# Kernel tuning notes

Measured on AMD Instinct MI355X. Metric: run time of the kernel, lower is better.

The kernel has to match this reference:

```python
import jax, jax.numpy as jnp
import numpy as np

NEG = -1e9

def setup_inputs() -> dict:
    key = jax.random.key(0)
    kx, kq, kk, kv, kbq, kbk, kbv = jax.random.split(key, 7)
    B, S, E, D = 4, 2048, 1024, 64
    x = jax.random.normal(kx, (B, S, E), dtype=jnp.float32)
    # causal mask, broadcast over batch (mask == 0 positions get -1e9)
    mask = jnp.broadcast_to(jnp.tril(jnp.ones((S, S), dtype=jnp.int32)), (B, S, S))
    scale = 1.0 / np.sqrt(E)
    Wq = jax.random.normal(kq, (E, D), dtype=jnp.float32) * scale
    Wk = jax.random.normal(kk, (E, D), dtype=jnp.float32) * scale
    Wv = jax.random.normal(kv, (E, D), dtype=jnp.float32) * scale
    bq = jnp.zeros((D,), dtype=jnp.float32)
    bk = jnp.zeros((D,), dtype=jnp.float32)
    bv = jnp.zeros((D,), dtype=jnp.float32)
    return {"x": x, "mask": mask, "Wq": Wq, "bq": bq, "Wk": Wk, "bk": bk, "Wv": Wv, "bv": bv}

def reference(x, mask, Wq, bq, Wk, bk, Wv, bv):
    # Faithful to original: forward passes (K(x), Q(x), V(x)) into sdpa,
    # so the K-projection plays the 'query' role and Q-projection the 'key' role.
    q = jnp.einsum('bse,ed->bsd', x, Wk) + bk  # K(x) used as queries
    k = jnp.einsum('bse,ed->bsd', x, Wq) + bq  # Q(x) used as keys
    v = jnp.einsum('bse,ed->bsd', x, Wv) + bv
    d = q.shape[-1]
    scores = jnp.einsum('bsd,btd->bst', q, k) / jnp.sqrt(jnp.asarray(d, q.dtype))
    scores = jnp.where(mask == 0, jnp.asarray(NEG, scores.dtype), scores)
    weights = jax.nn.softmax(scores, axis=-1)
    return jnp.einsum('bst,btd->bsd', weights, v)
```

## Files before the change

### kernel.cpp

```cpp
#include <hip/hip_runtime.h>

typedef short bf16x8 __attribute__((ext_vector_type(8)));
typedef float f32x4  __attribute__((ext_vector_type(4)));
typedef int   i32x4  __attribute__((ext_vector_type(4)));

#define NEG_BIG (-1e9f)

__device__ __forceinline__ float bf2f(unsigned short h){
  union { unsigned u; float f; } v; v.u = ((unsigned)h) << 16; return v.f;
}
__device__ __forceinline__ unsigned short f2bf(float f){
  union { float f; unsigned u; } v; v.f = f;
  unsigned u = v.u;
  return (unsigned short)((u + 0x7FFFu + ((u >> 16) & 1u)) >> 16);
}

__global__ __launch_bounds__(256) void prep_kernel(
    const float* __restrict__ Wq, const float* __restrict__ bq,
    const float* __restrict__ Wk, const float* __restrict__ bk,
    const float* __restrict__ Wv, const float* __restrict__ bv,
    unsigned short* __restrict__ Wimg, float* __restrict__ bias)
{
  __shared__ float Wt[64][65];

  const int tid = threadIdx.x;
  const int kb2 = blockIdx.x / 6;
  const int rem = blockIdx.x % 6;
  const int mat = rem >> 1;
  const int kh  = rem & 1;
  const int kbase = kb2 * 128 + kh * 64;

  const float* W = (mat == 0) ? Wk : (mat == 1) ? Wq : Wv;

  #pragma unroll
  for (int i = 0; i < 4; i++) {
    int krow = (tid >> 4) + i * 16;
    int d4   = (tid & 15) * 4;
    f32x4 v = *(const f32x4*)&W[(size_t)(kbase + krow) * 64 + d4];
    Wt[krow][d4 + 0] = v[0];
    Wt[krow][d4 + 1] = v[1];
    Wt[krow][d4 + 2] = v[2];
    Wt[krow][d4 + 3] = v[3];
  }
  __syncthreads();

  const int d = tid >> 2;
  const int c = tid & 3;
  const int r = mat * 64 + d;
  #pragma unroll
  for (int h = 0; h < 2; h++) {
    int cc = c + h * 4;
    bf16x8 o;
    #pragma unroll
    for (int i = 0; i < 8; i++) o[i] = f2bf(Wt[cc * 8 + i][d]);
    *(bf16x8*)&Wimg[(size_t)kb2 * 24576 + r * 128 + kh * 64 + cc * 8] = o;
  }

  if (blockIdx.x == 0 && tid < 192) {
    float b;
    if (tid < 64)       b = bk[tid];
    else if (tid < 128) b = bq[tid - 64];
    else                b = bv[tid - 128];
    bias[tid] = b;
  }
}

__global__ __launch_bounds__(256, 2) void proj_kernel(
    const float* __restrict__ x,
    const unsigned short* __restrict__ Wimg,
    const float* __restrict__ bias,
    unsigned short* __restrict__ Qh,
    unsigned short* __restrict__ Kh, unsigned short* __restrict__ Vth)
{
  __shared__ __align__(16) unsigned short Axb[32 * 128];
  __shared__ __align__(16) unsigned short Wc[96 * 128];

  const int tid  = threadIdx.x;
  const int lane = tid & 63;
  const int w    = tid >> 6;
  const int rh   = w & 1;
  const int cg   = w >> 1;
  const int quad = lane >> 4;
  const int li   = lane & 15;
  const int rowbase = (blockIdx.x >> 1) * 32;
  const int ch      = blockIdx.x & 1;

  const int xr0 = tid >> 4,          xc0 = tid & 15;
  const int xr1 = (tid + 256) >> 4,  xc1 = tid & 15;
  const float* agp0 = x + (size_t)(rowbase + xr0) * 1024 + xc0 * 8;
  const float* agp1 = x + (size_t)(rowbase + xr1) * 1024 + xc1 * 8;
  const int aslot0 = xr0 * 128 + (xc0 ^ (xr0 & 15)) * 8;
  const int aslot1 = xr1 * 128 + (xc1 ^ (xr1 & 15)) * 8;

  int wslot[6];
  const unsigned short* wgp[6];
  #pragma unroll
  for (int j = 0; j < 6; j++) {
    int cid = tid + j * 256;
    int wr = cid >> 4, c = cid & 15;
    wslot[j] = wr * 128 + (c ^ (wr & 15)) * 8;
    wgp[j] = Wimg + (size_t)(ch * 96 + wr) * 128 + c * 8;
  }

  f32x4 acc[3];
  #pragma unroll
  for (int c = 0; c < 3; c++) acc[c] = (f32x4){0.f, 0.f, 0.f, 0.f};

  const int alr = rh * 16 + li;

  f32x4 rA[4];
  rA[0] = *(const f32x4*)(agp0);
  rA[1] = *(const f32x4*)(agp0 + 4);
  rA[2] = *(const f32x4*)(agp1);
  rA[3] = *(const f32x4*)(agp1 + 4);
  i32x4 rW[6];
  #pragma unroll
  for (int j = 0; j < 6; j++) rW[j] = *(const i32x4*)(wgp[j]);

  for (int ks = 0; ks < 8; ks++) {
    bf16x8 xa, xb;
    #pragma unroll
    for (int j = 0; j < 4; j++) {
      xa[j]     = f2bf(rA[0][j]);
      xa[4 + j] = f2bf(rA[1][j]);
      xb[j]     = f2bf(rA[2][j]);
      xb[4 + j] = f2bf(rA[3][j]);
    }
    __syncthreads();
    *(bf16x8*)&Axb[aslot0] = xa;
    *(bf16x8*)&Axb[aslot1] = xb;
    #pragma unroll
    for (int j = 0; j < 6; j++) *(i32x4*)&Wc[wslot[j]] = rW[j];
    if (ks < 7) {
      rA[0] = *(const f32x4*)(agp0 + (ks + 1) * 128);
      rA[1] = *(const f32x4*)(agp0 + (ks + 1) * 128 + 4);
      rA[2] = *(const f32x4*)(agp1 + (ks + 1) * 128);
      rA[3] = *(const f32x4*)(agp1 + (ks + 1) * 128 + 4);
      #pragma unroll
      for (int j = 0; j < 6; j++)
        rW[j] = *(const i32x4*)(wgp[j] + (size_t)(ks + 1) * 24576);
    }
    __syncthreads();

    #pragma unroll
    for (int sub = 0; sub < 4; sub++) {
      bf16x8 af = *(const bf16x8*)&Axb[alr * 128 + ((sub * 4 + quad) ^ (alr & 15)) * 8];
      #pragma unroll
      for (int ct = 0; ct < 3; ct++) {
        const int lw = cg * 48 + ct * 16 + li;
        bf16x8 bf = *(const bf16x8*)&Wc[lw * 128 + ((sub * 4 + quad) ^ (lw & 15)) * 8];
        acc[ct] = __builtin_amdgcn_mfma_f32_16x16x32_bf16(af, bf, acc[ct], 0, 0, 0);
      }
    }
  }

  if (ch == 0) {
    #pragma unroll
    for (int ct = 0; ct < 3; ct++)
      #pragma unroll
      for (int r = 0; r < 4; r++) {
        int row = rowbase + rh * 16 + quad * 4 + r;
        int col = cg * 48 + ct * 16 + li;
        unsigned short h = f2bf(acc[ct][r] + bias[col]);
        if (col < 64) Qh[(size_t)row * 64 + col] = h;
        else          Kh[(size_t)row * 64 + (col - 64)] = h;
      }
  } else {
    __syncthreads();
    unsigned short* Vlds = Wc;
    #pragma unroll
    for (int ct = 0; ct < 3; ct++)
      #pragma unroll
      for (int r = 0; r < 4; r++) {
        int srow = rh * 16 + quad * 4 + r;
        int col = 96 + cg * 48 + ct * 16 + li;
        unsigned short h = f2bf(acc[ct][r] + bias[col]);
        if (col < 128) Kh[(size_t)(rowbase + srow) * 64 + (col - 64)] = h;
        else           Vlds[(col - 128) * 40 + srow] = h;
      }
    __syncthreads();
    const int d  = tid >> 2;
    const int sc = tid & 3;
    bf16x8 vv = *(const bf16x8*)&Vlds[d * 40 + sc * 8];
    const int grow = rowbase;
    const int bb = grow >> 11, s0 = (grow & 2047) + sc * 8;
    *(bf16x8*)&Vth[(size_t)bb * 131072 + (size_t)d * 2048 + s0] = vv;
  }
}

__global__ __launch_bounds__(256, 3) void attn_part_kernel(
    const unsigned short* __restrict__ Qh,
    const unsigned short* __restrict__ Kh,
    const unsigned short* __restrict__ Vth,
    float* __restrict__ pacc, float* __restrict__ pl,
    float* __restrict__ out)
{
  __shared__ __align__(16) unsigned short Kst[2][64 * 64];
  __shared__ __align__(16) unsigned short Vst[2][64 * 64];
  __shared__ __align__(16) unsigned short Ps[4][16 * 72];

  const int tid  = threadIdx.x;
  const int lane = tid & 63;
  const int w    = tid >> 6;
  const int quad = lane >> 4;
  const int li   = lane & 15;

  const int b = blockIdx.x / 187;
  int r = blockIdx.x % 187;
  int qg = 31, part = 0;
  #pragma unroll 1
  for (int g = 31; g >= 0; g--) {
    int Pg = (g + 3) / 3;
    if (r < Pg) { qg = g; part = r; break; }
    r -= Pg;
  }
  const int nkt = qg + 1;
  const int P   = (qg + 3) / 3;
  const int base = nkt / P, rem = nkt % P;
  const int kt0 = part * base + (part < rem ? part : rem);
  const int kt1 = kt0 + base + (part < rem ? 1 : 0);
  const int qbase = qg * 64 + w * 16;

  size_t qoff = ((size_t)(b * 2048 + qbase) + li) * 64 + quad * 8;
  bf16x8 qh0 = *(const bf16x8*)(Qh + qoff);
  bf16x8 qh1 = *(const bf16x8*)(Qh + qoff + 32);

  f32x4 acc[4];
  #pragma unroll
  for (int c = 0; c < 4; c++) acc[c] = (f32x4){0.f, 0.f, 0.f, 0.f};
  f32x4 lacc = (f32x4){0.f, 0.f, 0.f, 0.f};

  bf16x8 ones;
  #pragma unroll
  for (int j = 0; j < 8; j++) ones[j] = (short)0x3F80;

  const int srow = tid >> 2, sc = tid & 3;
  const unsigned short* kgp = Kh + (size_t)(b * 2048 + srow) * 64 + sc * 8;
  const unsigned short* vgp = Vth + (size_t)b * 131072 + (size_t)srow * 2048 + sc * 8;
  const int ks0 = srow * 64 + ((sc)     ^ (srow & 7)) * 8;
  const int ks1 = srow * 64 + ((sc + 4) ^ (srow & 7)) * 8;

  i32x4 rk0 = *(const i32x4*)(kgp + (size_t)kt0 * 4096);
  i32x4 rk1 = *(const i32x4*)(kgp + (size_t)kt0 * 4096 + 32);
  i32x4 rv0 = *(const i32x4*)(vgp + kt0 * 64);
  i32x4 rv1 = *(const i32x4*)(vgp + kt0 * 64 + 32);

  *(i32x4*)&Kst[0][ks0] = rk0;
  *(i32x4*)&Kst[0][ks1] = rk1;
  *(i32x4*)&Vst[0][ks0] = rv0;
  *(i32x4*)&Vst[0][ks1] = rv1;
  __syncthreads();

  int cur = 0;
  for (int kt = kt0; kt < kt1; kt++) {
    const bool more = (kt + 1 < kt1);
    if (more) {
      rk0 = *(const i32x4*)(kgp + (size_t)(kt + 1) * 4096);
      rk1 = *(const i32x4*)(kgp + (size_t)(kt + 1) * 4096 + 32);
      rv0 = *(const i32x4*)(vgp + (kt + 1) * 64);
      rv1 = *(const i32x4*)(vgp + (kt + 1) * 64 + 32);
    }

    f32x4 s[4];
    #pragma unroll
    for (int c = 0; c < 4; c++) s[c] = (f32x4){0.f, 0.f, 0.f, 0.f};
    __builtin_amdgcn_s_setprio(1);
    #pragma unroll
    for (int ct = 0; ct < 4; ct++) {
      const int n = ct * 16 + li;
      bf16x8 kf0 = *(const bf16x8*)&Kst[cur][n * 64 + ((quad)     ^ (n & 7)) * 8];
      bf16x8 kf1 = *(const bf16x8*)&Kst[cur][n * 64 + ((quad + 4) ^ (n & 7)) * 8];
      s[ct] = __builtin_amdgcn_mfma_f32_16x16x32_bf16(qh0, kf0, s[ct], 0, 0, 0);
      s[ct] = __builtin_amdgcn_mfma_f32_16x16x32_bf16(qh1, kf1, s[ct], 0, 0, 0);
    }
    __builtin_amdgcn_s_setprio(0);

    const bool diag = (kt == qg);
    const int kb = kt * 64;
    #pragma unroll
    for (int ct = 0; ct < 4; ct++)
      #pragma unroll
      for (int rr = 0; rr < 4; rr++) {
        float t = fmaf(s[ct][rr], 0.18033688011112042f, -23.083120654223414f);
        if (diag && (kb + ct * 16 + li > qbase + quad * 4 + rr)) t = -1e30f;
        Ps[w][(quad * 4 + rr) * 72 + ct * 16 + li] = f2bf(exp2f(t));
      }

    bf16x8 ap0 = *(const bf16x8*)&Ps[w][li * 72 + quad * 8];
    bf16x8 ap1 = *(const bf16x8*)&Ps[w][li * 72 + 32 + quad * 8];

    __builtin_amdgcn_s_setprio(1);
    lacc = __builtin_amdgcn_mfma_f32_16x16x32_bf16(ap0, ones, lacc, 0, 0, 0);
    lacc = __builtin_amdgcn_mfma_f32_16x16x32_bf16(ap1, ones, lacc, 0, 0, 0);
    #pragma unroll
    for (int ct = 0; ct < 4; ct++) {
      const int n = ct * 16 + li;
      bf16x8 vf0 = *(const bf16x8*)&Vst[cur][n * 64 + ((quad)     ^ (n & 7)) * 8];
      bf16x8 vf1 = *(const bf16x8*)&Vst[cur][n * 64 + ((quad + 4) ^ (n & 7)) * 8];
      acc[ct] = __builtin_amdgcn_mfma_f32_16x16x32_bf16(ap0, vf0, acc[ct], 0, 0, 0);
      acc[ct] = __builtin_amdgcn_mfma_f32_16x16x32_bf16(ap1, vf1, acc[ct], 0, 0, 0);
    }
    __builtin_amdgcn_s_setprio(0);

    if (more) {
      *(i32x4*)&Kst[cur ^ 1][ks0] = rk0;
      *(i32x4*)&Kst[cur ^ 1][ks1] = rk1;
      *(i32x4*)&Vst[cur ^ 1][ks0] = rv0;
      *(i32x4*)&Vst[cur ^ 1][ks1] = rv1;
      __syncthreads();
      cur ^= 1;
    }
  }

  if (P == 1) {
    float inv[4];
    #pragma unroll
    for (int rr = 0; rr < 4; rr++) inv[rr] = 1.0f / lacc[rr];
    #pragma unroll
    for (int ct = 0; ct < 4; ct++)
      #pragma unroll
      for (int rr = 0; rr < 4; rr++)
        out[(size_t)(b * 2048 + qg * 64 + w * 16 + quad * 4 + rr) * 64 + ct * 16 + li]
          = acc[ct][rr] * inv[rr];
    return;
  }

  const int slot = (b * 32 + qg) * 16 + part;
  float* pa = pacc + (size_t)slot * 4096;
  #pragma unroll
  for (int ct = 0; ct < 4; ct++)
    #pragma unroll
    for (int rr = 0; rr < 4; rr++)
      pa[(w * 16 + quad * 4 + rr) * 64 + ct * 16 + li] = acc[ct][rr];
  if (li == 0) {
    #pragma unroll
    for (int rr = 0; rr < 4; rr++)
      pl[slot * 64 + w * 16 + quad * 4 + rr] = lacc[rr];
  }
}

__global__ __launch_bounds__(256) void attn_merge_kernel(
    const float* __restrict__ pacc, const float* __restrict__ pl,
    float* __restrict__ out)
{
  const int tid = threadIdx.x;
  const int b   = blockIdx.x / 29;
  const int qg  = (blockIdx.x % 29) + 3;
  const int rr  = tid >> 2;
  const int c0  = (tid & 3) * 16;
  const int P   = (qg + 3) / 3;
  const int slot0 = (b * 32 + qg) * 16;

  f32x4 a0 = (f32x4){0.f,0.f,0.f,0.f}, a1 = a0, a2 = a0, a3 = a0;
  float L = 0.f;
  for (int p = 0; p < P; p++) {
    const float* pa = pacc + (size_t)(slot0 + p) * 4096 + rr * 64 + c0;
    a0 += *(const f32x4*)(pa);
    a1 += *(const f32x4*)(pa + 4);
    a2 += *(const f32x4*)(pa + 8);
    a3 += *(const f32x4*)(pa + 12);
    L += pl[(slot0 + p) * 64 + rr];
  }
  float inv = 1.f / L;
  float* o = out + ((size_t)(b * 2048 + qg * 64 + rr)) * 64 + c0;
  *(f32x4*)(o)      = a0 * inv;
  *(f32x4*)(o + 4)  = a1 * inv;
  *(f32x4*)(o + 8)  = a2 * inv;
  *(f32x4*)(o + 12) = a3 * inv;
}

extern "C" void kernel_launch(void* const* d_in, const int* in_sizes, int n_in,
                              void* d_out, int out_size, void* d_ws, size_t ws_size,
                              hipStream_t stream)
{
  (void)in_sizes; (void)n_in; (void)out_size; (void)ws_size;
  const float* x  = (const float*)d_in[0];
  const float* Wq = (const float*)d_in[2];
  const float* bq = (const float*)d_in[3];
  const float* Wk = (const float*)d_in[4];
  const float* bk = (const float*)d_in[5];
  const float* Wv = (const float*)d_in[6];
  const float* bv = (const float*)d_in[7];
  float* out = (float*)d_out;

  char* ws = (char*)d_ws;
  const size_t MB = 1u << 20;
  unsigned short* Qh   = (unsigned short*)(ws);
  unsigned short* Kh   = (unsigned short*)(ws + 2 * MB);
  unsigned short* Vth  = (unsigned short*)(ws + 4 * MB);
  unsigned short* Wimg = (unsigned short*)(ws + 6 * MB);
  float*          bias = (float*)(ws + 6 * MB + 786432);
  float*          pacc = (float*)(ws + 8 * MB);
  float*          pl   = (float*)(ws + 40 * MB);

  prep_kernel<<<dim3(48), dim3(256), 0, stream>>>(Wq, bq, Wk, bk, Wv, bv, Wimg, bias);
  proj_kernel<<<dim3(512), dim3(256), 0, stream>>>(x, Wimg, bias, Qh, Kh, Vth);
  attn_part_kernel<<<dim3(748), dim3(256), 0, stream>>>(Qh, Kh, Vth, pacc, pl, out);
  attn_merge_kernel<<<dim3(116), dim3(256), 0, stream>>>(pacc, pl, out);
}
```

Baseline: 149.9 us.

## Double-buffer projection tiles and load weights directly into LDS

The projection kernel now keeps two LDS buffers for the x and weight tiles, so the next k-step's loads are issued while MFMAs run on the current buffer, with one barrier per step instead of two. Weight tiles move global→LDS through global_load_lds, skipping the register round-trip. Since that instruction cannot swizzle on the way in, the prep kernel now writes the XOR swizzle into the weight image itself. The cost is double the LDS footprint, which may lower occupancy from the requested two blocks per CU, plus reliance on correct ordering and waits for the asynchronous LDS loads.

```diff
diff --git a/kernel.cpp b/kernel.cpp
--- a/kernel.cpp
+++ b/kernel.cpp
@@ -13,6 +13,12 @@
   union { float f; unsigned u; } v; v.f = f;
   unsigned u = v.u;
   return (unsigned short)((u + 0x7FFFu + ((u >> 16) & 1u)) >> 16);
+}
+
+__device__ __forceinline__ void gload_lds16(const unsigned short* g, unsigned short* l){
+  __builtin_amdgcn_global_load_lds(
+      (const __attribute__((address_space(1))) unsigned int*)g,
+      (__attribute__((address_space(3))) unsigned int*)l, 16, 0, 0);
 }
 
 __global__ __launch_bounds__(256) void prep_kernel(
@@ -50,10 +56,12 @@
   #pragma unroll
   for (int h = 0; h < 2; h++) {
     int cc = c + h * 4;
+    int cfull = kh * 8 + cc;
+    int cstore = cfull ^ (r & 15);
     bf16x8 o;
     #pragma unroll
     for (int i = 0; i < 8; i++) o[i] = f2bf(Wt[cc * 8 + i][d]);
-    *(bf16x8*)&Wimg[(size_t)kb2 * 24576 + r * 128 + kh * 64 + cc * 8] = o;
+    *(bf16x8*)&Wimg[(size_t)kb2 * 24576 + r * 128 + cstore * 8] = o;
   }
 
   if (blockIdx.x == 0 && tid < 192) {
@@ -72,8 +80,8 @@
     unsigned short* __restrict__ Qh,
     unsigned short* __restrict__ Kh, unsigned short* __restrict__ Vth)
 {
-  __shared__ __align__(16) unsigned short Axb[32 * 128];
-  __shared__ __align__(16) unsigned short Wc[96 * 128];
+  __shared__ __align__(16) unsigned short Axb[2][32 * 128];
+  __shared__ __align__(16) unsigned short Wc[2][96 * 128];
 
   const int tid  = threadIdx.x;
   const int lane = tid & 63;
@@ -92,15 +100,8 @@
   const int aslot0 = xr0 * 128 + (xc0 ^ (xr0 & 15)) * 8;
   const int aslot1 = xr1 * 128 + (xc1 ^ (xr1 & 15)) * 8;
 
-  int wslot[6];
-  const unsigned short* wgp[6];
-  #pragma unroll
-  for (int j = 0; j < 6; j++) {
-    int cid = tid + j * 256;
-    int wr = cid >> 4, c = cid & 15;
-    wslot[j] = wr * 128 + (c ^ (wr & 15)) * 8;
-    wgp[j] = Wimg + (size_t)(ch * 96 + wr) * 128 + c * 8;
-  }
+  const unsigned short* wtile = Wimg + (size_t)ch * 96 * 128;
+  const int wchunk = w * 64 + lane;
 
   f32x4 acc[3];
   #pragma unroll
@@ -113,11 +114,11 @@
   rA[1] = *(const f32x4*)(agp0 + 4);
   rA[2] = *(const f32x4*)(agp1);
   rA[3] = *(const f32x4*)(agp1 + 4);
-  i32x4 rW[6];
-  #pragma unroll
-  for (int j = 0; j < 6; j++) rW[j] = *(const i32x4*)(wgp[j]);
-
-  for (int ks = 0; ks < 8; ks++) {
+  #pragma unroll
+  for (int j = 0; j < 6; j++)
+    gload_lds16(wtile + (size_t)(j * 256 + wchunk) * 8,
+                &Wc[0][(j * 256 + w * 64) * 8]);
+  {
     bf16x8 xa, xb;
     #pragma unroll
     for (int j = 0; j < 4; j++) {
@@ -126,31 +127,50 @@
       xb[j]     = f2bf(rA[2][j]);
       xb[4 + j] = f2bf(rA[3][j]);
     }
-    __syncthreads();
-    *(bf16x8*)&Axb[aslot0] = xa;
-    *(bf16x8*)&Axb[aslot1] = xb;
-    #pragma unroll
-    for (int j = 0; j < 6; j++) *(i32x4*)&Wc[wslot[j]] = rW[j];
-    if (ks < 7) {
+    *(bf16x8*)&Axb[0][aslot0] = xa;
+    *(bf16x8*)&Axb[0][aslot1] = xb;
+  }
+  __syncthreads();
+
+  int cur = 0;
+  for (int ks = 0; ks < 8; ks++) {
+    const bool more = (ks < 7);
+    if (more) {
+      const unsigned short* wnext = wtile + (size_t)(ks + 1) * 24576;
+      #pragma unroll
+      for (int j = 0; j < 6; j++)
+        gload_lds16(wnext + (size_t)(j * 256 + wchunk) * 8,
+                    &Wc[cur ^ 1][(j * 256 + w * 64) * 8]);
       rA[0] = *(const f32x4*)(agp0 + (ks + 1) * 128);
       rA[1] = *(const f32x4*)(agp0 + (ks + 1) * 128 + 4);
       rA[2] = *(const f32x4*)(agp1 + (ks + 1) * 128);
       rA[3] = *(const f32x4*)(agp1 + (ks + 1) * 128 + 4);
-      #pragma unroll
-      for (int j = 0; j < 6; j++)
-        rW[j] = *(const i32x4*)(wgp[j] + (size_t)(ks + 1) * 24576);
-    }
-    __syncthreads();
+    }
 
     #pragma unroll
     for (int sub = 0; sub < 4; sub++) {
-      bf16x8 af = *(const bf16x8*)&Axb[alr * 128 + ((sub * 4 + quad) ^ (alr & 15)) * 8];
+      bf16x8 af = *(const bf16x8*)&Axb[cur][alr * 128 + ((sub * 4 + quad) ^ (alr & 15)) * 8];
       #pragma unroll
       for (int ct = 0; ct < 3; ct++) {
         const int lw = cg * 48 + ct * 16 + li;
-        bf16x8 bf = *(const bf16x8*)&Wc[lw * 128 + ((sub * 4 + quad) ^ (lw & 15)) * 8];
+        bf16x8 bf = *(const bf16x8*)&Wc[cur][lw * 128 + ((sub * 4 + quad) ^ (lw & 15)) * 8];
         acc[ct] = __builtin_amdgcn_mfma_f32_16x16x32_bf16(af, bf, acc[ct], 0, 0, 0);
       }
+    }
+
+    if (more) {
+      bf16x8 xa, xb;
+      #pragma unroll
+      for (int j = 0; j < 4; j++) {
+        xa[j]     = f2bf(rA[0][j]);
+        xa[4 + j] = f2bf(rA[1][j]);
+        xb[j]     = f2bf(rA[2][j]);
+        xb[4 + j] = f2bf(rA[3][j]);
+      }
+      *(bf16x8*)&Axb[cur ^ 1][aslot0] = xa;
+      *(bf16x8*)&Axb[cur ^ 1][aslot1] = xb;
+      __syncthreads();
+      cur ^= 1;
     }
   }
 
@@ -167,7 +187,7 @@
       }
   } else {
     __syncthreads();
-    unsigned short* Vlds = Wc;
+    unsigned short* Vlds = &Wc[0][0];
     #pragma unroll
     for (int ct = 0; ct < 3; ct++)
       #pragma unroll
```

Result: slower. 153.4 us (+2.3%).
